# Kernel tuning notes

Hardware: AMD Instinct MI355X
Metric: run time of the kernel (lower is better)

The kernel has to match this reference:

```python
import jax, jax.numpy as jnp
import numpy as np

NUM_HEADS = 8
EPS = 1e-12  # matches torch F.normalize eps


def setup_inputs() -> dict:
    key = jax.random.key(0)
    ks = jax.random.split(key, 4)
    B, C, H, W = 32, 384, 32, 32
    x = jax.random.normal(ks[0], (B, C, H, W), dtype=jnp.float32)
    w_qkv = jax.random.normal(ks[1], (3 * C, C), dtype=jnp.float32) * (1.0 / np.sqrt(C))
    b_qkv = jnp.zeros((3 * C,), dtype=jnp.float32)
    temperature = jnp.ones((NUM_HEADS, 1, 1), dtype=jnp.float32)
    w_proj = jax.random.normal(ks[2], (C, C), dtype=jnp.float32) * (1.0 / np.sqrt(C))
    b_proj = jnp.zeros((C,), dtype=jnp.float32)
    return {"x": x, "w_qkv": w_qkv, "b_qkv": b_qkv, "temperature": temperature,
            "w_proj": w_proj, "b_proj": b_proj}


def _l2norm_tokens(t):
    # L2-normalize over the token axis N (last dim), torch F.normalize semantics
    n = jnp.sqrt(jnp.sum(t * t, axis=-1, keepdims=True))
    return t / jnp.maximum(n, EPS)


def reference(x, w_qkv, b_qkv, temperature, w_proj, b_proj):
    B, C, H, W = x.shape
    N = H * W
    nh = NUM_HEADS
    dh = C // nh
    xf = x.reshape(B, C, N)
    # 1x1 conv == channel GEMM: [B,3C,N]
    qkv = jnp.einsum('oc,bcn->bon', w_qkv, xf) + b_qkv[:, None]
    qkv = qkv.reshape(B, 3, nh, dh, N)
    q, k, v = qkv[:, 0], qkv[:, 1], qkv[:, 2]  # each [B,nh,dh,N]
    q = _l2norm_tokens(q)
    k = _l2norm_tokens(k)
    # cross-covariance: contract over N -> small [B,nh,dh,dh]
    attn = jnp.einsum('bhdn,bhen->bhde', q, k) * temperature
    attn = jax.nn.softmax(attn, axis=-1)
    out = jnp.einsum('bhde,bhen->bhdn', attn, v).reshape(B, C, N)
    out = jnp.einsum('oc,bcn->bon', w_proj, out) + b_proj[:, None]
    return x + out.reshape(B, C, H, W)
```

## Files before the change

kernel.cpp:

```cpp
#include <hip/hip_runtime.h>
#include <hip/hip_bf16.h>
#include <stdint.h>

#define BATCH  32
#define CDIM   384
#define NTOK   1024
#define NHEADS 8
#define DH     48

using f32x4  = __attribute__((ext_vector_type(4))) float;
using bf16x8 = __attribute__((ext_vector_type(8))) short;
using u16x4  = __attribute__((ext_vector_type(4))) uint16_t;
using u16x8  = __attribute__((ext_vector_type(8))) uint16_t;

__device__ __forceinline__ uint16_t f2bf(float f) {
  uint32_t x = __float_as_uint(f);
  uint32_t r = (x + 0x7fffu + ((x >> 16) & 1u)) >> 16;
  return (uint16_t)r;
}
__device__ __forceinline__ float bf2f(uint16_t u) {
  return __uint_as_float(((uint32_t)u) << 16);
}

#define GLL16(gsrc, ldst)                                                    \
  __builtin_amdgcn_global_load_lds(                                          \
      (const __attribute__((address_space(1))) void*)(gsrc),                 \
      (__attribute__((address_space(3))) void*)(ldst), 16, 0, 0)

__global__ __launch_bounds__(256) void k_transpose_x(const float* __restrict__ x,
                                                     uint16_t* __restrict__ xT) {
  __shared__ float t[64][65];
  int tid = threadIdx.x;
  int n0 = blockIdx.x * 64;
  int c0 = blockIdx.y * 64;
  int b  = blockIdx.z;
  const float* xb = x + (size_t)b * CDIM * NTOK;
#pragma unroll
  for (int p = 0; p < 4; ++p) {
    int r  = (tid >> 4) + p * 16;
    int cc = (tid & 15) * 4;
    float4 v = *(const float4*)(xb + (size_t)(c0 + r) * NTOK + n0 + cc);
    t[r][cc + 0] = v.x; t[r][cc + 1] = v.y; t[r][cc + 2] = v.z; t[r][cc + 3] = v.w;
  }
  __syncthreads();
  uint16_t* xTb = xT + (size_t)b * NTOK * CDIM;
#pragma unroll
  for (int p = 0; p < 2; ++p) {
    int n  = (tid >> 3) + p * 32;
    int cb = (tid & 7) * 8;
    u16x8 o;
#pragma unroll
    for (int j = 0; j < 8; ++j) o[j] = f2bf(t[cb + j][n]);
    *(u16x8*)(xTb + (size_t)(n0 + n) * CDIM + c0 + cb) = o;
  }
}

__global__ __launch_bounds__(256) void k_convert_w(const float* __restrict__ wqkv,
                                                   const float* __restrict__ wproj,
                                                   uint16_t* __restrict__ wq,
                                                   uint16_t* __restrict__ wp) {
  int n1 = 3 * CDIM * CDIM;
  int n2 = CDIM * CDIM;
  int stride = gridDim.x * 256;
  for (int i = blockIdx.x * 256 + threadIdx.x; i < n1 + n2; i += stride) {
    if (i < n1) wq[i] = f2bf(wqkv[i]);
    else        wp[i - n1] = f2bf(wproj[i - n1]);
  }
}

__device__ __forceinline__ void stage64(const uint16_t* __restrict__ A,
                                        const uint16_t* __restrict__ B,
                                        uint16_t* lA, uint16_t* lB,
                                        int kt, int tid) {
#pragma unroll
  for (int iss = 0; iss < 4; ++iss) {
    int ch = tid + 256 * iss;
    int r  = ch >> 3;
    int cs = (((ch & 7) ^ (r & 7)) << 3);
    GLL16(A + (size_t)r * 384 + kt + cs, lA + (size_t)ch * 8);
    GLL16(B + (size_t)r * 384 + kt + cs, lB + (size_t)ch * 8);
  }
}

__device__ __forceinline__ void compute64(const uint16_t* lA, const uint16_t* lB,
                                          f32x4 acc[4][4],
                                          int wr, int wc, int lr, int g) {
#pragma unroll
  for (int ks = 0; ks < 2; ++ks) {
    bf16x8 af[4], bfr[4];
#pragma unroll
    for (int mt = 0; mt < 4; ++mt) {
      int row = wr * 64 + mt * 16 + lr;
      int sl  = (((ks * 4 + g) ^ (row & 7)) << 3);
      af[mt] = *(const bf16x8*)(lA + (size_t)row * 64 + sl);
    }
#pragma unroll
    for (int nt = 0; nt < 4; ++nt) {
      int row = wc * 64 + nt * 16 + lr;
      int sl  = (((ks * 4 + g) ^ (row & 7)) << 3);
      bfr[nt] = *(const bf16x8*)(lB + (size_t)row * 64 + sl);
    }
#pragma unroll
    for (int mt = 0; mt < 4; ++mt)
#pragma unroll
      for (int nt = 0; nt < 4; ++nt)
        acc[mt][nt] = __builtin_amdgcn_mfma_f32_16x16x32_bf16(af[mt], bfr[nt], acc[mt][nt], 0, 0, 0);
  }
}

__device__ __forceinline__ void gemm_tile_128(const uint16_t* __restrict__ A,
                                              const uint16_t* __restrict__ B,
                                              uint16_t* lds,
                                              f32x4 acc[4][4], int tid) {
  int w = tid >> 6, lane = tid & 63;
  int wr = w >> 1, wc = w & 1, lr = lane & 15, g = lane >> 4;
  uint16_t* A0 = lds;
  uint16_t* B0 = lds + 8192;
  uint16_t* A1 = lds + 16384;
  uint16_t* B1 = lds + 24576;

  stage64(A, B, A0, B0, 0, tid);
  asm volatile("s_waitcnt vmcnt(0)" ::: "memory");
  __builtin_amdgcn_s_barrier();
#pragma unroll
  for (int kt = 0; kt < 384; kt += 128) {
    if (kt + 64 < 384) stage64(A, B, A1, B1, kt + 64, tid);
    compute64(A0, B0, acc, wr, wc, lr, g);
    asm volatile("s_waitcnt vmcnt(0)" ::: "memory");
    __builtin_amdgcn_s_barrier();
    if (kt + 128 < 384) stage64(A, B, A0, B0, kt + 128, tid);
    if (kt + 64 < 384) compute64(A1, B1, acc, wr, wc, lr, g);
    asm volatile("s_waitcnt vmcnt(0)" ::: "memory");
    __builtin_amdgcn_s_barrier();
  }
}

__global__ __launch_bounds__(256) void k_qkv(const uint16_t* __restrict__ Wq,
                                             const uint16_t* __restrict__ xT,
                                             const float* __restrict__ bqkv,
                                             uint16_t* __restrict__ qk,
                                             uint16_t* __restrict__ vT) {
  __shared__ uint16_t lds[4 * 8192];
  int tid = threadIdx.x;
  int jt = blockIdx.x, bm = blockIdx.y;
  int o0 = bm * 128, j0 = jt * 128;
  f32x4 acc[4][4];
#pragma unroll
  for (int i = 0; i < 4; ++i)
#pragma unroll
    for (int j = 0; j < 4; ++j) acc[i][j] = (f32x4){0.f, 0.f, 0.f, 0.f};

  gemm_tile_128(Wq + (size_t)o0 * 384, xT + (size_t)j0 * 384, lds, acc, tid);

  int w = tid >> 6, lane = tid & 63;
  int wr = w >> 1, wc = w & 1, lr = lane & 15, g = lane >> 4;
#pragma unroll
  for (int mt = 0; mt < 4; ++mt) {
    int ob = o0 + wr * 64 + mt * 16 + g * 4;
    float b0 = bqkv[ob + 0], b1 = bqkv[ob + 1], b2 = bqkv[ob + 2], b3 = bqkv[ob + 3];
#pragma unroll
    for (int nt = 0; nt < 4; ++nt) {
      int j = j0 + wc * 64 + nt * 16 + lr;
      int b = j >> 10, n = j & 1023;
      f32x4 v = acc[mt][nt];
      float v0 = v[0] + b0, v1 = v[1] + b1, v2 = v[2] + b2, v3 = v[3] + b3;
      if (ob < 768) {
        uint16_t* dst = qk + ((size_t)(b * 768 + ob) * 1024 + n);
        dst[0] = f2bf(v0); dst[1024] = f2bf(v1); dst[2048] = f2bf(v2); dst[3072] = f2bf(v3);
      } else {
        int oc = ob - 768;
        int h = oc / 48, d = oc % 48;
        u16x4 p;
        p[0] = f2bf(v0); p[1] = f2bf(v1); p[2] = f2bf(v2); p[3] = f2bf(v3);
        *(u16x4*)(vT + ((size_t)((b * 8 + h) * 1024 + n) * 48 + d)) = p;
      }
    }
  }
}

__global__ __launch_bounds__(256) void k_attn(const uint16_t* __restrict__ qk,
                                              const uint16_t* __restrict__ vT,
                                              const float* __restrict__ temperature,
                                              uint16_t* __restrict__ aT) {
  __shared__ float Sp[4][48][49];
  __shared__ float Sf[48][49];
  __shared__ uint16_t P[48][72];
  __shared__ float nrm[96];
  int tid = threadIdx.x, w = tid >> 6, lane = tid & 63;
  int bh = blockIdx.x, b = bh >> 3, h = bh & 7;
  const uint16_t* qbase = qk + (size_t)(b * 768 + h * 48) * 1024;
  const uint16_t* kbase = qbase + (size_t)384 * 1024;

  for (int r = w; r < 96; r += 4) {
    const uint16_t* row = (r < 48) ? (qbase + (size_t)r * 1024)
                                   : (kbase + (size_t)(r - 48) * 1024);
    float s = 0.f;
#pragma unroll
    for (int jj = 0; jj < 4; ++jj) {
      u16x4 u = *(const u16x4*)(row + (size_t)(jj * 64 + lane) * 4);
#pragma unroll
      for (int e = 0; e < 4; ++e) { float f = bf2f(u[e]); s += f * f; }
    }
#pragma unroll
    for (int off = 32; off > 0; off >>= 1) s += __shfl_down(s, off);
    if (lane == 0) nrm[r] = fmaxf(sqrtf(s), 1e-12f);
  }

  int lr = lane & 15, g = lane >> 4;
  int nbase = w * 256;
  f32x4 sacc[3][3];
#pragma unroll
  for (int i = 0; i < 3; ++i)
#pragma unroll
    for (int j = 0; j < 3; ++j) sacc[i][j] = (f32x4){0.f, 0.f, 0.f, 0.f};
#pragma unroll
  for (int ks = 0; ks < 8; ++ks) {
    bf16x8 aq[3], bk[3];
#pragma unroll
    for (int mt = 0; mt < 3; ++mt)
      aq[mt] = *(const bf16x8*)(qbase + (size_t)(mt * 16 + lr) * 1024 + nbase + ks * 32 + g * 8);
#pragma unroll
    for (int et = 0; et < 3; ++et)
      bk[et] = *(const bf16x8*)(kbase + (size_t)(et * 16 + lr) * 1024 + nbase + ks * 32 + g * 8);
#pragma unroll
    for (int mt = 0; mt < 3; ++mt)
#pragma unroll
      for (int et = 0; et < 3; ++et)
        sacc[mt][et] = __builtin_amdgcn_mfma_f32_16x16x32_bf16(aq[mt], bk[et], sacc[mt][et], 0, 0, 0);
  }
#pragma unroll
  for (int mt = 0; mt < 3; ++mt)
#pragma unroll
    for (int et = 0; et < 3; ++et)
#pragma unroll
      for (int r = 0; r < 4; ++r)
        Sp[w][mt * 16 + g * 4 + r][et * 16 + lr] = sacc[mt][et][r];
  __syncthreads();

  float temp = temperature[h];
  for (int idx = tid; idx < 48 * 48; idx += 256) {
    int d = idx / 48, e = idx - d * 48;
    float s = Sp[0][d][e] + Sp[1][d][e] + Sp[2][d][e] + Sp[3][d][e];
    Sf[d][e] = s * temp / (nrm[d] * nrm[48 + e]);
  }
  __syncthreads();

  if (tid < 48) {
    int d = tid;
    float m = -1e30f;
    for (int e = 0; e < 48; ++e) m = fmaxf(m, Sf[d][e]);
    float sum = 0.f;
    for (int e = 0; e < 48; ++e) { float v = __expf(Sf[d][e] - m); sum += v; Sf[d][e] = v; }
    float inv = 1.f / sum;
    for (int e = 0; e < 48; ++e) P[d][e] = f2bf(Sf[d][e] * inv);
    for (int e = 48; e < 64; ++e) P[d][e] = 0;
  }
  __syncthreads();

  bf16x8 af[3][2];
#pragma unroll
  for (int mt = 0; mt < 3; ++mt)
#pragma unroll
    for (int ks = 0; ks < 2; ++ks)
      af[mt][ks] = *(const bf16x8*)(&P[mt * 16 + lr][ks * 32 + g * 8]);
  const uint16_t* vb = vT + (size_t)(b * 8 + h) * 1024 * 48;
  bf16x8 zf;
#pragma unroll
  for (int i = 0; i < 8; ++i) zf[i] = 0;
#pragma unroll 4
  for (int nt = 0; nt < 16; ++nt) {
    int n = w * 256 + nt * 16 + lr;
    bf16x8 bv[2];
    bv[0] = *(const bf16x8*)(vb + (size_t)n * 48 + g * 8);
    int eb1 = 32 + g * 8;
    bv[1] = (eb1 < 48) ? *(const bf16x8*)(vb + (size_t)n * 48 + eb1) : zf;
    f32x4 o[3];
#pragma unroll
    for (int mt = 0; mt < 3; ++mt) o[mt] = (f32x4){0.f, 0.f, 0.f, 0.f};
#pragma unroll
    for (int ks = 0; ks < 2; ++ks)
#pragma unroll
      for (int mt = 0; mt < 3; ++mt)
        o[mt] = __builtin_amdgcn_mfma_f32_16x16x32_bf16(af[mt][ks], bv[ks], o[mt], 0, 0, 0);
#pragma unroll
    for (int mt = 0; mt < 3; ++mt) {
      int c = h * 48 + mt * 16 + g * 4;
      u16x4 p;
#pragma unroll
      for (int r = 0; r < 4; ++r) p[r] = f2bf(o[mt][r]);
      *(u16x4*)(aT + ((size_t)(b * 1024 + n) * 384 + c)) = p;
    }
  }
}

__global__ __launch_bounds__(256) void k_proj(const uint16_t* __restrict__ Wp,
                                              const uint16_t* __restrict__ aT,
                                              const float* __restrict__ bproj,
                                              const float* __restrict__ x,
                                              float* __restrict__ out) {
  __shared__ uint16_t lds[4 * 8192];
  int tid = threadIdx.x;
  int jt = blockIdx.x, bm = blockIdx.y;
  int o0 = bm * 128, j0 = jt * 128;
  f32x4 acc[4][4];
#pragma unroll
  for (int i = 0; i < 4; ++i)
#pragma unroll
    for (int j = 0; j < 4; ++j) acc[i][j] = (f32x4){0.f, 0.f, 0.f, 0.f};

  gemm_tile_128(Wp + (size_t)o0 * 384, aT + (size_t)j0 * 384, lds, acc, tid);

  int w = tid >> 6, lane = tid & 63;
  int wr = w >> 1, wc = w & 1, lr = lane & 15, g = lane >> 4;
#pragma unroll
  for (int mt = 0; mt < 4; ++mt) {
    int ob = o0 + wr * 64 + mt * 16 + g * 4;
    float b0 = bproj[ob + 0], b1 = bproj[ob + 1], b2 = bproj[ob + 2], b3 = bproj[ob + 3];
#pragma unroll
    for (int nt = 0; nt < 4; ++nt) {
      int j = j0 + wc * 64 + nt * 16 + lr;
      int b = j >> 10, n = j & 1023;
      f32x4 v = acc[mt][nt];
      size_t i0 = (size_t)(b * 384 + ob) * 1024 + n;
      out[i0]        = v[0] + b0 + x[i0];
      out[i0 + 1024] = v[1] + b1 + x[i0 + 1024];
      out[i0 + 2048] = v[2] + b2 + x[i0 + 2048];
      out[i0 + 3072] = v[3] + b3 + x[i0 + 3072];
    }
  }
}

extern "C" void kernel_launch(void* const* d_in, const int* in_sizes, int n_in,
                              void* d_out, int out_size, void* d_ws, size_t ws_size,
                              hipStream_t stream) {
  const float* x     = (const float*)d_in[0];
  const float* wqkv  = (const float*)d_in[1];
  const float* bqkv  = (const float*)d_in[2];
  const float* temp  = (const float*)d_in[3];
  const float* wproj = (const float*)d_in[4];
  const float* bproj = (const float*)d_in[5];
  float* out = (float*)d_out;

  char* ws = (char*)d_ws;
  size_t off = 0;
  auto alloc = [&](size_t bytes) -> char* {
    char* p = ws + off;
    off += (bytes + 255) & ~(size_t)255;
    return p;
  };
  uint16_t* xT    = (uint16_t*)alloc((size_t)BATCH * NTOK * CDIM * 2);
  uint16_t* wq_bf = (uint16_t*)alloc((size_t)3 * CDIM * CDIM * 2);
  uint16_t* wp_bf = (uint16_t*)alloc((size_t)CDIM * CDIM * 2);
  uint16_t* qkbuf = (uint16_t*)alloc((size_t)BATCH * 768 * NTOK * 2);
  uint16_t* vTbuf = (uint16_t*)alloc((size_t)BATCH * NHEADS * NTOK * DH * 2);
  uint16_t* aT    = xT;

  k_transpose_x<<<dim3(NTOK / 64, CDIM / 64, BATCH), dim3(256), 0, stream>>>(x, xT);
  k_convert_w<<<dim3(576), dim3(256), 0, stream>>>(wqkv, wproj, wq_bf, wp_bf);
  k_qkv<<<dim3(256, 9), dim3(256), 0, stream>>>(wq_bf, xT, bqkv, qkbuf, vTbuf);
  k_attn<<<dim3(256), dim3(256), 0, stream>>>(qkbuf, vTbuf, temp, aT);
  k_proj<<<dim3(256, 3), dim3(256), 0, stream>>>(wp_bf, aT, bproj, x, out);
}
```

Baseline: 131.8 us.

## Shrink GEMM K-tile to 32 and overlap loads with partial vmcnt waits

```diff
diff --git a/kernel.cpp b/kernel.cpp
--- a/kernel.cpp
+++ b/kernel.cpp
@@ -68,44 +68,39 @@
   }
 }
 
-__device__ __forceinline__ void stage64(const uint16_t* __restrict__ A,
+__device__ __forceinline__ void stage32(const uint16_t* __restrict__ A,
                                         const uint16_t* __restrict__ B,
                                         uint16_t* lA, uint16_t* lB,
                                         int kt, int tid) {
 #pragma unroll
-  for (int iss = 0; iss < 4; ++iss) {
-    int ch = tid + 256 * iss;
-    int r  = ch >> 3;
-    int cs = (((ch & 7) ^ (r & 7)) << 3);
+  for (int i = 0; i < 2; ++i) {
+    int ch = tid + 256 * i;
+    int r  = ch >> 2;
+    int cs = (((ch & 3) ^ (r & 3)) << 3);
     GLL16(A + (size_t)r * 384 + kt + cs, lA + (size_t)ch * 8);
     GLL16(B + (size_t)r * 384 + kt + cs, lB + (size_t)ch * 8);
   }
 }
 
-__device__ __forceinline__ void compute64(const uint16_t* lA, const uint16_t* lB,
+__device__ __forceinline__ void compute32(const uint16_t* lA, const uint16_t* lB,
                                           f32x4 acc[4][4],
                                           int wr, int wc, int lr, int g) {
-#pragma unroll
-  for (int ks = 0; ks < 2; ++ks) {
-    bf16x8 af[4], bfr[4];
-#pragma unroll
-    for (int mt = 0; mt < 4; ++mt) {
-      int row = wr * 64 + mt * 16 + lr;
-      int sl  = (((ks * 4 + g) ^ (row & 7)) << 3);
-      af[mt] = *(const bf16x8*)(lA + (size_t)row * 64 + sl);
-    }
-#pragma unroll
-    for (int nt = 0; nt < 4; ++nt) {
-      int row = wc * 64 + nt * 16 + lr;
-      int sl  = (((ks * 4 + g) ^ (row & 7)) << 3);
-      bfr[nt] = *(const bf16x8*)(lB + (size_t)row * 64 + sl);
-    }
-#pragma unroll
-    for (int mt = 0; mt < 4; ++mt)
-#pragma unroll
-      for (int nt = 0; nt < 4; ++nt)
-        acc[mt][nt] = __builtin_amdgcn_mfma_f32_16x16x32_bf16(af[mt], bfr[nt], acc[mt][nt], 0, 0, 0);
-  }
+  bf16x8 af[4], bfr[4];
+#pragma unroll
+  for (int mt = 0; mt < 4; ++mt) {
+    int row = wr * 64 + mt * 16 + lr;
+    af[mt] = *(const bf16x8*)(lA + (size_t)row * 32 + ((g ^ (row & 3)) << 3));
+  }
+#pragma unroll
+  for (int nt = 0; nt < 4; ++nt) {
+    int row = wc * 64 + nt * 16 + lr;
+    bfr[nt] = *(const bf16x8*)(lB + (size_t)row * 32 + ((g ^ (row & 3)) << 3));
+  }
+#pragma unroll
+  for (int mt = 0; mt < 4; ++mt)
+#pragma unroll
+    for (int nt = 0; nt < 4; ++nt)
+      acc[mt][nt] = __builtin_amdgcn_mfma_f32_16x16x32_bf16(af[mt], bfr[nt], acc[mt][nt], 0, 0, 0);
 }
 
 __device__ __forceinline__ void gemm_tile_128(const uint16_t* __restrict__ A,
@@ -115,23 +110,23 @@
   int w = tid >> 6, lane = tid & 63;
   int wr = w >> 1, wc = w & 1, lr = lane & 15, g = lane >> 4;
   uint16_t* A0 = lds;
-  uint16_t* B0 = lds + 8192;
-  uint16_t* A1 = lds + 16384;
-  uint16_t* B1 = lds + 24576;
-
-  stage64(A, B, A0, B0, 0, tid);
-  asm volatile("s_waitcnt vmcnt(0)" ::: "memory");
-  __builtin_amdgcn_s_barrier();
-#pragma unroll
-  for (int kt = 0; kt < 384; kt += 128) {
-    if (kt + 64 < 384) stage64(A, B, A1, B1, kt + 64, tid);
-    compute64(A0, B0, acc, wr, wc, lr, g);
-    asm volatile("s_waitcnt vmcnt(0)" ::: "memory");
-    __builtin_amdgcn_s_barrier();
-    if (kt + 128 < 384) stage64(A, B, A0, B0, kt + 128, tid);
-    if (kt + 64 < 384) compute64(A1, B1, acc, wr, wc, lr, g);
-    asm volatile("s_waitcnt vmcnt(0)" ::: "memory");
-    __builtin_amdgcn_s_barrier();
+  uint16_t* B0 = lds + 4096;
+  uint16_t* A1 = lds + 8192;
+  uint16_t* B1 = lds + 12288;
+
+  stage32(A, B, A0, B0, 0, tid);
+  stage32(A, B, A1, B1, 32, tid);
+#pragma unroll
+  for (int t = 0; t < 12; ++t) {
+    if (t < 10) asm volatile("s_waitcnt vmcnt(4)\n\ts_barrier" ::: "memory");
+    else        asm volatile("s_waitcnt vmcnt(0)\n\ts_barrier" ::: "memory");
+    if (t & 1) compute32(A1, B1, acc, wr, wc, lr, g);
+    else       compute32(A0, B0, acc, wr, wc, lr, g);
+    asm volatile("s_barrier" ::: "memory");
+    if (t < 10) {
+      if (t & 1) stage32(A, B, A1, B1, (t + 2) * 32, tid);
+      else       stage32(A, B, A0, B0, (t + 2) * 32, tid);
+    }
   }
 }
 
@@ -140,7 +135,7 @@
                                              const float* __restrict__ bqkv,
                                              uint16_t* __restrict__ qk,
                                              uint16_t* __restrict__ vT) {
-  __shared__ uint16_t lds[4 * 8192];
+  __shared__ uint16_t lds[16384];
   int tid = threadIdx.x;
   int jt = blockIdx.x, bm = blockIdx.y;
   int o0 = bm * 128, j0 = jt * 128;
@@ -298,7 +293,7 @@
                                               const float* __restrict__ bproj,
                                               const float* __restrict__ x,
                                               float* __restrict__ out) {
-  __shared__ uint16_t lds[4 * 8192];
+  __shared__ uint16_t lds[16384];
   int tid = threadIdx.x;
   int jt = blockIdx.x, bm = blockIdx.y;
   int o0 = bm * 128, j0 = jt * 128;
```

After: 130.3 us. About the same (-1.1%).
